# Kernel tuning notes

Hardware: AMD Instinct MI355X
Metric: run time of the kernel (lower is better)

## Reference

```python
import jax, jax.numpy as jnp
import numpy as np

N_NODES = 40000
N_EDGES = 640000
IN_F = 128
HID = 128
N_GRAPHS = 64
N_CLASSES = 2
EPS = 1e-5


def gcn_conv(h_in, W, b, row, col, n):
    # h' = D^-1/2 (A + I) D^-1/2 (X W) + b  (PyG GCNConv with self-loops)
    h = h_in @ W  # [N, out]
    loop = jnp.arange(n, dtype=row.dtype)
    r = jnp.concatenate([row, loop])
    c = jnp.concatenate([col, loop])
    deg = jax.ops.segment_sum(jnp.ones_like(c, dtype=h.dtype), c, num_segments=n)
    dinv = jnp.where(deg > 0, jax.lax.rsqrt(deg), 0.0)
    norm = dinv[r] * dinv[c]  # [E+N]
    msgs = h[r] * norm[:, None]  # gather + scale
    out = jax.ops.segment_sum(msgs, c, num_segments=n)  # scatter-add
    return out + b


def batch_norm(x, gamma, beta):
    mu = jnp.mean(x, axis=0)
    var = jnp.mean(jnp.square(x - mu), axis=0)  # biased, as torch BN
    return gamma * (x - mu) * jax.lax.rsqrt(var + EPS) + beta


def setup_inputs() -> dict:
    key = jax.random.key(0)
    ks = jax.random.split(key, 12)
    s = 1.0 / np.sqrt(HID)
    return {
        "x": jax.random.normal(ks[0], (N_NODES, IN_F), dtype=jnp.float32),
        "edge_index": jax.random.randint(ks[1], (2, N_EDGES), 0, N_NODES, dtype=jnp.int32),
        "batch": jnp.sort(jax.random.randint(ks[2], (N_NODES,), 0, N_GRAPHS, dtype=jnp.int32)),
        "W1": jax.random.normal(ks[3], (IN_F, HID), dtype=jnp.float32) * s,
        "b1": jnp.zeros((HID,), dtype=jnp.float32),
        "W2": jax.random.normal(ks[4], (HID, HID), dtype=jnp.float32) * s,
        "b2": jnp.zeros((HID,), dtype=jnp.float32),
        "gamma1": jnp.ones((HID,), dtype=jnp.float32),
        "beta1": jnp.zeros((HID,), dtype=jnp.float32),
        "gamma2": jnp.ones((HID,), dtype=jnp.float32),
        "beta2": jnp.zeros((HID,), dtype=jnp.float32),
        "lin1_W": jax.random.normal(ks[5], (HID, HID // 2), dtype=jnp.float32) * s,
        "lin1_b": jnp.zeros((HID // 2,), dtype=jnp.float32),
        "lin2_W": jax.random.normal(ks[6], (HID // 2, N_CLASSES), dtype=jnp.float32) * s,
        "lin2_b": jnp.zeros((N_CLASSES,), dtype=jnp.float32),
    }


def reference(x, edge_index, batch, W1, b1, W2, b2, gamma1, beta1, gamma2, beta2,
              lin1_W, lin1_b, lin2_W, lin2_b):
    row, col = edge_index[0], edge_index[1]
    # layer 1: GCNConv -> BN -> ReLU (dropout = identity in eval)
    h = gcn_conv(x, W1, b1, row, col, N_NODES)
    h = jax.nn.relu(batch_norm(h, gamma1, beta1))
    # layer 2
    h = gcn_conv(h, W2, b2, row, col, N_NODES)
    h = jax.nn.relu(batch_norm(h, gamma2, beta2))
    # global mean pool over graphs
    sums = jax.ops.segment_sum(h, batch, num_segments=N_GRAPHS)
    cnt = jax.ops.segment_sum(jnp.ones((N_NODES,), dtype=h.dtype), batch, num_segments=N_GRAPHS)
    pooled = sums / jnp.maximum(cnt, 1.0)[:, None]  # [G, HID]
    z = jax.nn.relu(pooled @ lin1_W + lin1_b)
    return z @ lin2_W + lin2_b  # [G, num_classes]
```

## Files before the change

kernel.cpp:

```cpp
#include <hip/hip_runtime.h>
#include <hip/hip_fp16.h>

#define NN 40000
#define NE 640000
#define F 128
#define NG 64
#define SCAN_NB 157

typedef _Float16 f16x8 __attribute__((ext_vector_type(8)));
typedef float f32x4 __attribute__((ext_vector_type(4)));

union U4H {
    uint4 u;
    f16x8 h;
};

__global__ __launch_bounds__(256) void k_init(const int* __restrict__ batch, int* __restrict__ deg,
                                              float* __restrict__ pooled, float* __restrict__ slabs,
                                              int* __restrict__ gstart, int* __restrict__ gend) {
    int i = blockIdx.x * 256 + threadIdx.x;
    if (i < NN) {
        deg[i] = 0;
        int g = batch[i];
        if (i == 0 || batch[i - 1] != g) gstart[g] = i;
        if (i == NN - 1 || batch[i + 1] != g) gend[g] = i + 1;
    }
    if (i < NG * F) pooled[i] = 0.f;
    if (i < 64 * 128) {
        slabs[i] = 0.f;
        slabs[8192 + i] = 0.f;
        slabs[16384 + i] = 0.f;
        slabs[24576 + i] = 0.f;
    }
}

__global__ __launch_bounds__(256) void k_deg(const int* __restrict__ col, int* __restrict__ deg) {
    int e = blockIdx.x * 256 + threadIdx.x;
    if (e < NE) atomicAdd(&deg[col[e]], 1);
}

__global__ __launch_bounds__(256) void k_scan1(const int* __restrict__ deg, int* __restrict__ partial) {
    __shared__ int sp[256];
    int t = threadIdx.x;
    int i = blockIdx.x * 256 + t;
    sp[t] = (i < NN) ? deg[i] : 0;
    __syncthreads();
#pragma unroll
    for (int off = 128; off > 0; off >>= 1) {
        if (t < off) sp[t] += sp[t + off];
        __syncthreads();
    }
    if (t == 0) partial[blockIdx.x] = sp[0];
}

__global__ __launch_bounds__(256) void k_scan2(const int* __restrict__ partial, int* __restrict__ bsum,
                                               int* __restrict__ indptr) {
    __shared__ int sp[256];
    int t = threadIdx.x;
    int v = (t < SCAN_NB) ? partial[t] : 0;
    sp[t] = v;
    __syncthreads();
#pragma unroll
    for (int off = 1; off < 256; off <<= 1) {
        int add = (t >= off) ? sp[t - off] : 0;
        __syncthreads();
        sp[t] += add;
        __syncthreads();
    }
    if (t < SCAN_NB) bsum[t] = sp[t] - v;
    if (t == SCAN_NB - 1) indptr[NN] = sp[t];
}

__global__ __launch_bounds__(256) void k_scan3(const int* __restrict__ deg, const int* __restrict__ bsum,
                                               int* __restrict__ indptr, int* __restrict__ cursor,
                                               float* __restrict__ dinv) {
    __shared__ int sd[256];
    int t = threadIdx.x;
    int i = blockIdx.x * 256 + t;
    int d = (i < NN) ? deg[i] : 0;
    sd[t] = d;
    __syncthreads();
#pragma unroll
    for (int off = 1; off < 256; off <<= 1) {
        int add = (t >= off) ? sd[t - off] : 0;
        __syncthreads();
        sd[t] += add;
        __syncthreads();
    }
    if (i < NN) {
        int excl = bsum[blockIdx.x] + sd[t] - d;
        indptr[i] = excl;
        cursor[i] = excl;
        dinv[i] = rsqrtf((float)(d + 1));
    }
}

__global__ __launch_bounds__(256) void k_fill(const int* __restrict__ row, const int* __restrict__ col,
                                              int* __restrict__ cursor, int* __restrict__ esrc) {
    int e = blockIdx.x * 256 + threadIdx.x;
    if (e < NE) {
        int c = col[e];
        int slot = atomicAdd(&cursor[c], 1);
        esrc[slot] = row[e];
    }
}

__global__ __launch_bounds__(256) void k_wprep(const float* __restrict__ W1, const float* __restrict__ W2,
                                               _Float16* __restrict__ img1, _Float16* __restrict__ img2) {
    int i = blockIdx.x * 256 + threadIdx.x;
    const float* W = (i < 16384) ? W1 : W2;
    _Float16* img = (i < 16384) ? img1 : img2;
    int j = i & 16383;
    int k = j >> 7, c = j & 127;
    float v = W[j];
    _Float16 h = (_Float16)v;
    _Float16 lo = (_Float16)(v - (float)h);
    int idx = (c * 128 + k) ^ ((c & 7) << 3);
    img[idx] = h;
    img[16384 + idx] = lo;
}

template <int MODE>
__global__ __launch_bounds__(256) void k_mgemm(const void* __restrict__ Ain, const uint4* __restrict__ wimg,
                                               const float* __restrict__ ss, const float* __restrict__ dinv,
                                               unsigned short* __restrict__ G) {
    __shared__ _Float16 WT[2][16384];
    int t = threadIdx.x;
    {
        uint4* dst = (uint4*)&WT[0][0];
#pragma unroll
        for (int i = 0; i < 16; i++) dst[i * 256 + t] = wimg[i * 256 + t];
    }
    __syncthreads();
    int w = t >> 6, l = t & 63;
    int r0w = blockIdx.x * 64 + w * 16;
    int lrow = l & 15, lk = l >> 4;
    int arow = r0w + lrow;

    U4H ah[4], al[4];
    if (MODE == 0) {
        const float* A = (const float*)Ain;
#pragma unroll
        for (int kk = 0; kk < 4; kk++) {
            int k0 = kk * 32 + lk * 8;
            float4 f0 = *(const float4*)&A[arow * 128 + k0];
            float4 f1 = *(const float4*)&A[arow * 128 + k0 + 4];
            float v[8] = {f0.x, f0.y, f0.z, f0.w, f1.x, f1.y, f1.z, f1.w};
#pragma unroll
            for (int j = 0; j < 8; j++) {
                _Float16 h = (_Float16)v[j];
                ah[kk].h[j] = h;
                al[kk].h[j] = (_Float16)(v[j] - (float)h);
            }
        }
    } else {
        const unsigned int* A = (const unsigned int*)Ain;
#pragma unroll
        for (int kk = 0; kk < 4; kk++) {
            int k0 = kk * 32 + lk * 8;
            uint4 u = *(const uint4*)&A[arow * 64 + (k0 >> 1)];
            unsigned int uu[4] = {u.x, u.y, u.z, u.w};
#pragma unroll
            for (int p = 0; p < 4; p++) {
                __half2 hp = *(__half2*)&uu[p];
                int k = k0 + 2 * p;
                float v0 = fmaxf(fmaf(__low2float(hp), ss[k], ss[128 + k]), 0.f);
                float v1 = fmaxf(fmaf(__high2float(hp), ss[k + 1], ss[129 + k]), 0.f);
                _Float16 h0 = (_Float16)v0;
                _Float16 h1 = (_Float16)v1;
                ah[kk].h[2 * p] = h0;
                ah[kk].h[2 * p + 1] = h1;
                al[kk].h[2 * p] = (_Float16)(v0 - (float)h0);
                al[kk].h[2 * p + 1] = (_Float16)(v1 - (float)h1);
            }
        }
    }

    f32x4 acc[8];
#pragma unroll
    for (int ct = 0; ct < 8; ct++) acc[ct] = (f32x4){0.f, 0.f, 0.f, 0.f};

#pragma unroll
    for (int kk = 0; kk < 4; kk++) {
        int k0 = kk * 32 + lk * 8;
#pragma unroll
        for (int ct = 0; ct < 8; ct++) {
            int c = ct * 16 + lrow;
            int idx = (c * 128 + k0) ^ ((c & 7) << 3);
            U4H bh, bl;
            bh.h = *(f16x8*)&WT[0][idx];
            bl.h = *(f16x8*)&WT[1][idx];
            acc[ct] = __builtin_amdgcn_mfma_f32_16x16x32_f16(ah[kk].h, bh.h, acc[ct], 0, 0, 0);
            acc[ct] = __builtin_amdgcn_mfma_f32_16x16x32_f16(al[kk].h, bh.h, acc[ct], 0, 0, 0);
            acc[ct] = __builtin_amdgcn_mfma_f32_16x16x32_f16(ah[kk].h, bl.h, acc[ct], 0, 0, 0);
        }
    }

    float dv[4];
#pragma unroll
    for (int j = 0; j < 4; j++) dv[j] = dinv[r0w + lk * 4 + j];
#pragma unroll
    for (int ct = 0; ct < 8; ct++) {
        int c = ct * 16 + lrow;
#pragma unroll
        for (int j = 0; j < 4; j++) {
            int r = r0w + lk * 4 + j;
            __half hv = __float2half(acc[ct][j] * dv[j]);
            G[r * 128 + c] = *(unsigned short*)&hv;
        }
    }
}

__device__ __forceinline__ void accum8(float* acc, uint4 u) {
    __half2 p0 = *(__half2*)&u.x, p1 = *(__half2*)&u.y, p2 = *(__half2*)&u.z, p3 = *(__half2*)&u.w;
    acc[0] += __low2float(p0); acc[1] += __high2float(p0);
    acc[2] += __low2float(p1); acc[3] += __high2float(p1);
    acc[4] += __low2float(p2); acc[5] += __high2float(p2);
    acc[6] += __low2float(p3); acc[7] += __high2float(p3);
}

__global__ __launch_bounds__(256) void k_agg(const uint4* __restrict__ g16, const int* __restrict__ indptr,
                                             const int* __restrict__ esrc, const float* __restrict__ dinv,
                                             const float* __restrict__ bias, uint4* __restrict__ hout,
                                             float* __restrict__ slabS, float* __restrict__ slabQ) {
    __shared__ float lsS[4][128];
    __shared__ float lsQ[4][128];
    int t = threadIdx.x;
    int w = t >> 6, l = t & 63;
    int slot = l >> 4, lc = l & 15;
    int v = blockIdx.x * 4 + w;
    int s = indptr[v], e = indptr[v + 1];
    float acc[8];
#pragma unroll
    for (int j = 0; j < 8; j++) acc[j] = 0.f;

    int i = s;
    for (; i + 15 < e; i += 16) {
        int r0 = esrc[i + slot];
        int r1 = esrc[i + 4 + slot];
        int r2 = esrc[i + 8 + slot];
        int r3 = esrc[i + 12 + slot];
        uint4 u0 = g16[r0 * 16 + lc];
        uint4 u1 = g16[r1 * 16 + lc];
        uint4 u2 = g16[r2 * 16 + lc];
        uint4 u3 = g16[r3 * 16 + lc];
        accum8(acc, u0);
        accum8(acc, u1);
        accum8(acc, u2);
        accum8(acc, u3);
    }
    for (; i + 3 < e; i += 4) {
        int r0 = esrc[i + slot];
        uint4 u0 = g16[r0 * 16 + lc];
        accum8(acc, u0);
    }
    if (i + slot < e) {
        int r0 = esrc[i + slot];
        uint4 u0 = g16[r0 * 16 + lc];
        accum8(acc, u0);
    }
#pragma unroll
    for (int j = 0; j < 8; j++) {
        acc[j] += __shfl_xor(acc[j], 16, 64);
        acc[j] += __shfl_xor(acc[j], 32, 64);
    }
    if (l < 16) {
        uint4 us = g16[v * 16 + l];
        accum8(acc, us);
        float dvv = dinv[l >= 0 ? v : 0];
        float4 ba = ((const float4*)bias)[2 * l];
        float4 bb = ((const float4*)bias)[2 * l + 1];
        float vv[8];
        vv[0] = acc[0] * dvv + ba.x; vv[1] = acc[1] * dvv + ba.y;
        vv[2] = acc[2] * dvv + ba.z; vv[3] = acc[3] * dvv + ba.w;
        vv[4] = acc[4] * dvv + bb.x; vv[5] = acc[5] * dvv + bb.y;
        vv[6] = acc[6] * dvv + bb.z; vv[7] = acc[7] * dvv + bb.w;
        __half2 h0 = __floats2half2_rn(vv[0], vv[1]);
        __half2 h1 = __floats2half2_rn(vv[2], vv[3]);
        __half2 h2 = __floats2half2_rn(vv[4], vv[5]);
        __half2 h3 = __floats2half2_rn(vv[6], vv[7]);
        uint4 o;
        o.x = *(unsigned int*)&h0; o.y = *(unsigned int*)&h1;
        o.z = *(unsigned int*)&h2; o.w = *(unsigned int*)&h3;
        hout[v * 16 + l] = o;
#pragma unroll
        for (int j = 0; j < 8; j++) {
            lsS[w][l * 8 + j] = vv[j];
            lsQ[w][l * 8 + j] = vv[j] * vv[j];
        }
    }
    __syncthreads();
    int sb = (blockIdx.x & 63) * 128;
    if (t < 128) {
        float v4 = (lsS[0][t] + lsS[1][t]) + (lsS[2][t] + lsS[3][t]);
        atomicAdd(&slabS[sb + t], v4);
    } else {
        int c = t - 128;
        float v4 = (lsQ[0][c] + lsQ[1][c]) + (lsQ[2][c] + lsQ[3][c]);
        atomicAdd(&slabQ[sb + c], v4);
    }
}

__global__ void k_finalize(const float* __restrict__ slabS, const float* __restrict__ slabQ,
                           const float* __restrict__ gamma, const float* __restrict__ beta,
                           float* __restrict__ ss) {
    int c = threadIdx.x;
    float s = 0.f, q = 0.f;
    for (int b = 0; b < 64; b++) {
        s += slabS[b * 128 + c];
        q += slabQ[b * 128 + c];
    }
    float mu = s * (1.f / NN);
    float var = q * (1.f / NN) - mu * mu;
    float sc = gamma[c] * rsqrtf(var + 1e-5f);
    ss[c] = sc;
    ss[128 + c] = beta[c] - mu * sc;
}

__global__ __launch_bounds__(256) void k_pool(const unsigned int* __restrict__ h, const int* __restrict__ batch,
                                              const float* __restrict__ ss, float* __restrict__ pooled) {
    int t = threadIdx.x, c2 = t & 63, q = t >> 6;
    float sc0 = ss[2 * c2], sc1 = ss[2 * c2 + 1];
    float sh0 = ss[128 + 2 * c2], sh1 = ss[129 + 2 * c2];
    int r0 = blockIdx.x * 64;
    int g_cur = -1;
    float a0 = 0.f, a1 = 0.f;
    for (int i = 0; i < 16; i++) {
        int r = r0 + q + 4 * i;
        int g = batch[r];
        unsigned int u = h[r * 64 + c2];
        __half2 p = *(__half2*)&u;
        float v0 = fmaxf(fmaf(__low2float(p), sc0, sh0), 0.f);
        float v1 = fmaxf(fmaf(__high2float(p), sc1, sh1), 0.f);
        if (g != g_cur) {
            if (g_cur >= 0) {
                atomicAdd(&pooled[g_cur * 128 + 2 * c2], a0);
                atomicAdd(&pooled[g_cur * 128 + 2 * c2 + 1], a1);
            }
            a0 = 0.f; a1 = 0.f; g_cur = g;
        }
        a0 += v0; a1 += v1;
    }
    if (g_cur >= 0) {
        atomicAdd(&pooled[g_cur * 128 + 2 * c2], a0);
        atomicAdd(&pooled[g_cur * 128 + 2 * c2 + 1], a1);
    }
}

__global__ __launch_bounds__(256) void k_head(const float* __restrict__ pooled, const int* __restrict__ gstart,
                                              const int* __restrict__ gend, const float* __restrict__ l1W,
                                              const float* __restrict__ l1b, const float* __restrict__ l2W,
                                              const float* __restrict__ l2b, float* __restrict__ out) {
    __shared__ float P[64 * 128];
    __shared__ float Z[64 * 64];
    int t = threadIdx.x;
    for (int i = t; i < 64 * 128; i += 256) {
        int g = i >> 7;
        float cnt = (float)max(gend[g] - gstart[g], 1);
        P[i] = pooled[i] / cnt;
    }
    __syncthreads();
    for (int o = t; o < 64 * 64; o += 256) {
        int g = o >> 6, j = o & 63;
        float s = l1b[j];
        for (int k = 0; k < 128; k++) s += P[g * 128 + k] * l1W[k * 64 + j];
        Z[o] = fmaxf(s, 0.f);
    }
    __syncthreads();
    if (t < 128) {
        int g = t >> 1, cls = t & 1;
        float s = l2b[cls];
        for (int k = 0; k < 64; k++) s += Z[g * 64 + k] * l2W[k * 2 + cls];
        out[g * 2 + cls] = s;
    }
}

extern "C" void kernel_launch(void* const* d_in, const int* in_sizes, int n_in, void* d_out, int out_size,
                              void* d_ws, size_t ws_size, hipStream_t stream) {
    (void)in_sizes; (void)n_in; (void)out_size; (void)ws_size;
    const float* x = (const float*)d_in[0];
    const int* ei = (const int*)d_in[1];
    const int* row = ei;
    const int* col = ei + NE;
    const int* batch = (const int*)d_in[2];
    const float* W1 = (const float*)d_in[3];
    const float* b1 = (const float*)d_in[4];
    const float* W2 = (const float*)d_in[5];
    const float* b2 = (const float*)d_in[6];
    const float* g1 = (const float*)d_in[7];
    const float* be1 = (const float*)d_in[8];
    const float* g2 = (const float*)d_in[9];
    const float* be2 = (const float*)d_in[10];
    const float* l1W = (const float*)d_in[11];
    const float* l1b = (const float*)d_in[12];
    const float* l2W = (const float*)d_in[13];
    const float* l2b = (const float*)d_in[14];
    float* out = (float*)d_out;

    char* ws = (char*)d_ws;
    size_t off = 0;
    auto alloc = [&](size_t bytes) {
        void* p = ws + off;
        off += (bytes + 255) & ~(size_t)255;
        return p;
    };
    unsigned int* g16 = (unsigned int*)alloc(NN * 64 * 4);
    unsigned int* h16a = (unsigned int*)alloc(NN * 64 * 4);
    unsigned int* h16b = (unsigned int*)alloc(NN * 64 * 4);
    int* deg = (int*)alloc(NN * 4);
    float* dinv = (float*)alloc(NN * 4);
    int* indptr = (int*)alloc((NN + 1) * 4);
    int* cursor = (int*)alloc(NN * 4);
    int* esrc = (int*)alloc(NE * 4);
    int* partial = (int*)alloc(256 * 4);
    int* bsum = (int*)alloc(256 * 4);
    float* slabs = (float*)alloc(4 * 64 * 128 * 4);
    float* ss1 = (float*)alloc(256 * 4);
    float* ss2 = (float*)alloc(256 * 4);
    float* pooled = (float*)alloc(NG * F * 4);
    int* gstart = (int*)alloc(NG * 4);
    int* gend = (int*)alloc(NG * 4);
    _Float16* wimg1 = (_Float16*)alloc(32768 * 2);
    _Float16* wimg2 = (_Float16*)alloc(32768 * 2);

    float* slab1S = slabs;
    float* slab1Q = slabs + 8192;
    float* slab2S = slabs + 16384;
    float* slab2Q = slabs + 24576;

    k_init<<<SCAN_NB, 256, 0, stream>>>(batch, deg, pooled, slabs, gstart, gend);
    k_wprep<<<128, 256, 0, stream>>>(W1, W2, wimg1, wimg2);
    k_deg<<<NE / 256, 256, 0, stream>>>(col, deg);
    k_scan1<<<SCAN_NB, 256, 0, stream>>>(deg, partial);
    k_scan2<<<1, 256, 0, stream>>>(partial, bsum, indptr);
    k_scan3<<<SCAN_NB, 256, 0, stream>>>(deg, bsum, indptr, cursor, dinv);
    k_fill<<<NE / 256, 256, 0, stream>>>(row, col, cursor, esrc);

    k_mgemm<0><<<NN / 64, 256, 0, stream>>>(x, (const uint4*)wimg1, nullptr, dinv, (unsigned short*)g16);
    k_agg<<<NN / 4, 256, 0, stream>>>((const uint4*)g16, indptr, esrc, dinv, b1, (uint4*)h16a, slab1S, slab1Q);
    k_finalize<<<1, 128, 0, stream>>>(slab1S, slab1Q, g1, be1, ss1);

    k_mgemm<1><<<NN / 64, 256, 0, stream>>>(h16a, (const uint4*)wimg2, ss1, dinv, (unsigned short*)g16);
    k_agg<<<NN / 4, 256, 0, stream>>>((const uint4*)g16, indptr, esrc, dinv, b2, (uint4*)h16b, slab2S, slab2Q);
    k_finalize<<<1, 128, 0, stream>>>(slab2S, slab2Q, g2, be2, ss2);

    k_pool<<<NN / 64, 256, 0, stream>>>(h16b, batch, ss2, pooled);
    k_head<<<1, 256, 0, stream>>>(pooled, gstart, gend, l1W, l1b, l2W, l2b, out);
}
```

Baseline: 206.6 us.

## Split feature matrices into two 64-column planes and use 16-bit edge sources

The fp16 node-feature buffers are stored as two planes of 64 columns instead of one 128-column row. The aggregation kernel runs twice as many blocks, each handling one plane, with 8 edges per wave step instead of 4. Edge source indices are stored as unsigned short, which halves the CSR index traffic. The aim is a smaller gather working set per pass for better cache locality and more parallelism. The cost is that each edge list is read twice, and node ids above 65535 would break, which is safe only because NN=40000.

```diff
diff --git a/kernel.cpp b/kernel.cpp
--- a/kernel.cpp
+++ b/kernel.cpp
@@ -26,12 +26,7 @@
         if (i == NN - 1 || batch[i + 1] != g) gend[g] = i + 1;
     }
     if (i < NG * F) pooled[i] = 0.f;
-    if (i < 64 * 128) {
-        slabs[i] = 0.f;
-        slabs[8192 + i] = 0.f;
-        slabs[16384 + i] = 0.f;
-        slabs[24576 + i] = 0.f;
-    }
+    if (i < 32768) slabs[i] = 0.f;
 }
 
 __global__ __launch_bounds__(256) void k_deg(const int* __restrict__ col, int* __restrict__ deg) {
@@ -96,12 +91,12 @@
 }
 
 __global__ __launch_bounds__(256) void k_fill(const int* __restrict__ row, const int* __restrict__ col,
-                                              int* __restrict__ cursor, int* __restrict__ esrc) {
+                                              int* __restrict__ cursor, unsigned short* __restrict__ esrc) {
     int e = blockIdx.x * 256 + threadIdx.x;
     if (e < NE) {
         int c = col[e];
         int slot = atomicAdd(&cursor[c], 1);
-        esrc[slot] = row[e];
+        esrc[slot] = (unsigned short)row[e];
     }
 }
 
@@ -154,24 +149,25 @@
             }
         }
     } else {
-        const unsigned int* A = (const unsigned int*)Ain;
+        const uint4* A4 = (const uint4*)Ain;
 #pragma unroll
         for (int kk = 0; kk < 4; kk++) {
             int k0 = kk * 32 + lk * 8;
-            uint4 u = *(const uint4*)&A[arow * 64 + (k0 >> 1)];
+            int p = k0 >> 6, off = (k0 & 63) >> 3;
+            uint4 u = A4[(p * NN + arow) * 8 + off];
             unsigned int uu[4] = {u.x, u.y, u.z, u.w};
 #pragma unroll
-            for (int p = 0; p < 4; p++) {
-                __half2 hp = *(__half2*)&uu[p];
-                int k = k0 + 2 * p;
+            for (int pp = 0; pp < 4; pp++) {
+                __half2 hp = *(__half2*)&uu[pp];
+                int k = k0 + 2 * pp;
                 float v0 = fmaxf(fmaf(__low2float(hp), ss[k], ss[128 + k]), 0.f);
                 float v1 = fmaxf(fmaf(__high2float(hp), ss[k + 1], ss[129 + k]), 0.f);
                 _Float16 h0 = (_Float16)v0;
                 _Float16 h1 = (_Float16)v1;
-                ah[kk].h[2 * p] = h0;
-                ah[kk].h[2 * p + 1] = h1;
-                al[kk].h[2 * p] = (_Float16)(v0 - (float)h0);
-                al[kk].h[2 * p + 1] = (_Float16)(v1 - (float)h1);
+                ah[kk].h[2 * pp] = h0;
+                ah[kk].h[2 * pp + 1] = h1;
+                al[kk].h[2 * pp] = (_Float16)(v0 - (float)h0);
+                al[kk].h[2 * pp + 1] = (_Float16)(v1 - (float)h1);
             }
         }
     }
@@ -202,11 +198,12 @@
 #pragma unroll
     for (int ct = 0; ct < 8; ct++) {
         int c = ct * 16 + lrow;
+        int p = c >> 6, pc = c & 63;
 #pragma unroll
         for (int j = 0; j < 4; j++) {
             int r = r0w + lk * 4 + j;
             __half hv = __float2half(acc[ct][j] * dv[j]);
-            G[r * 128 + c] = *(unsigned short*)&hv;
+            G[(p * NN + r) * 64 + pc] = *(unsigned short*)&hv;
         }
     }
 }
@@ -219,16 +216,21 @@
     acc[6] += __low2float(p3); acc[7] += __high2float(p3);
 }
 
-__global__ __launch_bounds__(256) void k_agg(const uint4* __restrict__ g16, const int* __restrict__ indptr,
-                                             const int* __restrict__ esrc, const float* __restrict__ dinv,
-                                             const float* __restrict__ bias, uint4* __restrict__ hout,
-                                             float* __restrict__ slabS, float* __restrict__ slabQ) {
-    __shared__ float lsS[4][128];
-    __shared__ float lsQ[4][128];
+__global__ __launch_bounds__(256) void k_agg(const uint4* __restrict__ gP, const int* __restrict__ indptr,
+                                             const unsigned short* __restrict__ esrc,
+                                             const float* __restrict__ dinv, const float4* __restrict__ bias4,
+                                             uint4* __restrict__ houtP, float* __restrict__ slabS,
+                                             float* __restrict__ slabQ) {
+    __shared__ float lsS[4][64];
+    __shared__ float lsQ[4][64];
+    int bid = blockIdx.x;
+    int plane = (bid >> 2) & 1;
+    int nodeblk = (bid >> 3) * 4 + (bid & 3);
     int t = threadIdx.x;
     int w = t >> 6, l = t & 63;
-    int slot = l >> 4, lc = l & 15;
-    int v = blockIdx.x * 4 + w;
+    int lc = l & 7, slot = l >> 3;
+    int v = nodeblk * 4 + w;
+    const uint4* gp = gP + plane * (NN * 8);
     int s = indptr[v], e = indptr[v + 1];
     float acc[8];
 #pragma unroll
@@ -237,39 +239,34 @@
     int i = s;
     for (; i + 15 < e; i += 16) {
         int r0 = esrc[i + slot];
-        int r1 = esrc[i + 4 + slot];
-        int r2 = esrc[i + 8 + slot];
-        int r3 = esrc[i + 12 + slot];
-        uint4 u0 = g16[r0 * 16 + lc];
-        uint4 u1 = g16[r1 * 16 + lc];
-        uint4 u2 = g16[r2 * 16 + lc];
-        uint4 u3 = g16[r3 * 16 + lc];
+        int r1 = esrc[i + 8 + slot];
+        uint4 u0 = gp[r0 * 8 + lc];
+        uint4 u1 = gp[r1 * 8 + lc];
         accum8(acc, u0);
         accum8(acc, u1);
-        accum8(acc, u2);
-        accum8(acc, u3);
-    }
-    for (; i + 3 < e; i += 4) {
+    }
+    for (; i + 7 < e; i += 8) {
         int r0 = esrc[i + slot];
-        uint4 u0 = g16[r0 * 16 + lc];
+        uint4 u0 = gp[r0 * 8 + lc];
         accum8(acc, u0);
     }
     if (i + slot < e) {
         int r0 = esrc[i + slot];
-        uint4 u0 = g16[r0 * 16 + lc];
+        uint4 u0 = gp[r0 * 8 + lc];
         accum8(acc, u0);
     }
 #pragma unroll
     for (int j = 0; j < 8; j++) {
+        acc[j] += __shfl_xor(acc[j], 8, 64);
         acc[j] += __shfl_xor(acc[j], 16, 64);
         acc[j] += __shfl_xor(acc[j], 32, 64);
     }
-    if (l < 16) {
-        uint4 us = g16[v * 16 + l];
+    if (slot == 0) {
+        uint4 us = gp[v * 8 + lc];
         accum8(acc, us);
-        float dvv = dinv[l >= 0 ? v : 0];
-        float4 ba = ((const float4*)bias)[2 * l];
-        float4 bb = ((const float4*)bias)[2 * l + 1];
+        float dvv = dinv[v];
+        float4 ba = bias4[plane * 16 + lc * 2];
+        float4 bb = bias4[plane * 16 + lc * 2 + 1];
         float vv[8];
         vv[0] = acc[0] * dvv + ba.x; vv[1] = acc[1] * dvv + ba.y;
         vv[2] = acc[2] * dvv + ba.z; vv[3] = acc[3] * dvv + ba.w;
@@ -282,22 +279,20 @@
         uint4 o;
         o.x = *(unsigned int*)&h0; o.y = *(unsigned int*)&h1;
         o.z = *(unsigned int*)&h2; o.w = *(unsigned int*)&h3;
-        hout[v * 16 + l] = o;
+        houtP[(plane * NN + v) * 8 + lc] = o;
 #pragma unroll
         for (int j = 0; j < 8; j++) {
-            lsS[w][l * 8 + j] = vv[j];
-            lsQ[w][l * 8 + j] = vv[j] * vv[j];
-        }
-    }
-    __syncthreads();
-    int sb = (blockIdx.x & 63) * 128;
-    if (t < 128) {
-        float v4 = (lsS[0][t] + lsS[1][t]) + (lsS[2][t] + lsS[3][t]);
-        atomicAdd(&slabS[sb + t], v4);
-    } else {
-        int c = t - 128;
-        float v4 = (lsQ[0][c] + lsQ[1][c]) + (lsQ[2][c] + lsQ[3][c]);
-        atomicAdd(&slabQ[sb + c], v4);
+            lsS[w][lc * 8 + j] = vv[j];
+            lsQ[w][lc * 8 + j] = vv[j] * vv[j];
+        }
+    }
+    __syncthreads();
+    int sb = plane * 4096 + ((bid >> 3) & 63) * 64;
+    if (t < 64) {
+        atomicAdd(&slabS[sb + t], (lsS[0][t] + lsS[1][t]) + (lsS[2][t] + lsS[3][t]));
+    } else if (t < 128) {
+        int c = t - 64;
+        atomicAdd(&slabQ[sb + c], (lsQ[0][c] + lsQ[1][c]) + (lsQ[2][c] + lsQ[3][c]));
     }
 }
 
@@ -305,10 +300,11 @@
                            const float* __restrict__ gamma, const float* __restrict__ beta,
                            float* __restrict__ ss) {
     int c = threadIdx.x;
+    int plane = c >> 6, col = c & 63;
     float s = 0.f, q = 0.f;
     for (int b = 0; b < 64; b++) {
-        s += slabS[b * 128 + c];
-        q += slabQ[b * 128 + c];
+        s += slabS[plane * 4096 + b * 64 + col];
+        q += slabQ[plane * 4096 + b * 64 + col];
     }
     float mu = s * (1.f / NN);
     float var = q * (1.f / NN) - mu * mu;
@@ -320,6 +316,7 @@
 __global__ __launch_bounds__(256) void k_pool(const unsigned int* __restrict__ h, const int* __restrict__ batch,
                                               const float* __restrict__ ss, float* __restrict__ pooled) {
     int t = threadIdx.x, c2 = t & 63, q = t >> 6;
+    int p = c2 >> 5, pc = c2 & 31;
     float sc0 = ss[2 * c2], sc1 = ss[2 * c2 + 1];
     float sh0 = ss[128 + 2 * c2], sh1 = ss[129 + 2 * c2];
     int r0 = blockIdx.x * 64;
@@ -328,10 +325,10 @@
     for (int i = 0; i < 16; i++) {
         int r = r0 + q + 4 * i;
         int g = batch[r];
-        unsigned int u = h[r * 64 + c2];
-        __half2 p = *(__half2*)&u;
-        float v0 = fmaxf(fmaf(__low2float(p), sc0, sh0), 0.f);
-        float v1 = fmaxf(fmaf(__high2float(p), sc1, sh1), 0.f);
+        unsigned int u = h[(p * NN + r) * 32 + pc];
+        __half2 pr = *(__half2*)&u;
+        float v0 = fmaxf(fmaf(__low2float(pr), sc0, sh0), 0.f);
+        float v1 = fmaxf(fmaf(__high2float(pr), sc1, sh1), 0.f);
         if (g != g_cur) {
             if (g_cur >= 0) {
                 atomicAdd(&pooled[g_cur * 128 + 2 * c2], a0);
@@ -411,10 +408,10 @@
     float* dinv = (float*)alloc(NN * 4);
     int* indptr = (int*)alloc((NN + 1) * 4);
     int* cursor = (int*)alloc(NN * 4);
-    int* esrc = (int*)alloc(NE * 4);
+    unsigned short* esrc = (unsigned short*)alloc(NE * 2);
     int* partial = (int*)alloc(256 * 4);
     int* bsum = (int*)alloc(256 * 4);
-    float* slabs = (float*)alloc(4 * 64 * 128 * 4);
+    float* slabs = (float*)alloc(4 * 8192 * 4);
     float* ss1 = (float*)alloc(256 * 4);
     float* ss2 = (float*)alloc(256 * 4);
     float* pooled = (float*)alloc(NG * F * 4);
@@ -437,11 +434,13 @@
     k_fill<<<NE / 256, 256, 0, stream>>>(row, col, cursor, esrc);
 
     k_mgemm<0><<<NN / 64, 256, 0, stream>>>(x, (const uint4*)wimg1, nullptr, dinv, (unsigned short*)g16);
-    k_agg<<<NN / 4, 256, 0, stream>>>((const uint4*)g16, indptr, esrc, dinv, b1, (uint4*)h16a, slab1S, slab1Q);
+    k_agg<<<NN / 2, 256, 0, stream>>>((const uint4*)g16, indptr, esrc, dinv, (const float4*)b1,
+                                      (uint4*)h16a, slab1S, slab1Q);
     k_finalize<<<1, 128, 0, stream>>>(slab1S, slab1Q, g1, be1, ss1);
 
     k_mgemm<1><<<NN / 64, 256, 0, stream>>>(h16a, (const uint4*)wimg2, ss1, dinv, (unsigned short*)g16);
-    k_agg<<<NN / 4, 256, 0, stream>>>((const uint4*)g16, indptr, esrc, dinv, b2, (uint4*)h16b, slab2S, slab2Q);
+    k_agg<<<NN / 2, 256, 0, stream>>>((const uint4*)g16, indptr, esrc, dinv, (const float4*)b2,
+                                      (uint4*)h16b, slab2S, slab2Q);
     k_finalize<<<1, 128, 0, stream>>>(slab2S, slab2Q, g2, be2, ss2);
 
     k_pool<<<NN / 64, 256, 0, stream>>>(h16b, batch, ss2, pooled);
```

Measured after the change: 217.1 us. 1.05x slower.

## Fuse small setup kernels and BN finalize into neighbors, shrink edge indices

Applied to the files above, without the earlier changes.

Folds the weight-image prep into the init kernel, merges the single-block partial-sum scan into every block of the final scan, and has each GEMM/pool block recompute the BatchNorm scale/shift from the slabs instead of running a separate finalize kernel. This removes four small launches and their serialization gaps. It also stores edge source indices as 16-bit, which halves that gather traffic. The cost is redundant per-block reduction work (64-slab sums in every block). The 16-bit indices rely on node ids fitting in 65535, which holds for 40000 nodes.

```diff
diff --git a/kernel.cpp b/kernel.cpp
--- a/kernel.cpp
+++ b/kernel.cpp
@@ -17,7 +17,9 @@
 
 __global__ __launch_bounds__(256) void k_init(const int* __restrict__ batch, int* __restrict__ deg,
                                               float* __restrict__ pooled, float* __restrict__ slabs,
-                                              int* __restrict__ gstart, int* __restrict__ gend) {
+                                              int* __restrict__ gstart, int* __restrict__ gend,
+                                              const float* __restrict__ W1, const float* __restrict__ W2,
+                                              _Float16* __restrict__ img1, _Float16* __restrict__ img2) {
     int i = blockIdx.x * 256 + threadIdx.x;
     if (i < NN) {
         deg[i] = 0;
@@ -26,11 +28,18 @@
         if (i == NN - 1 || batch[i + 1] != g) gend[g] = i + 1;
     }
     if (i < NG * F) pooled[i] = 0.f;
-    if (i < 64 * 128) {
-        slabs[i] = 0.f;
-        slabs[8192 + i] = 0.f;
-        slabs[16384 + i] = 0.f;
-        slabs[24576 + i] = 0.f;
+    if (i < 32768) slabs[i] = 0.f;
+    if (i < 32768) {
+        const float* W = (i < 16384) ? W1 : W2;
+        _Float16* img = (i < 16384) ? img1 : img2;
+        int j = i & 16383;
+        int k = j >> 7, c = j & 127;
+        float v = W[j];
+        _Float16 h = (_Float16)v;
+        _Float16 lo = (_Float16)(v - (float)h);
+        int idx = (c * 128 + k) ^ ((c & 7) << 3);
+        img[idx] = h;
+        img[16384 + idx] = lo;
     }
 }
 
@@ -53,12 +62,13 @@
     if (t == 0) partial[blockIdx.x] = sp[0];
 }
 
-__global__ __launch_bounds__(256) void k_scan2(const int* __restrict__ partial, int* __restrict__ bsum,
-                                               int* __restrict__ indptr) {
+__global__ __launch_bounds__(256) void k_scan3(const int* __restrict__ deg, const int* __restrict__ partial,
+                                               int* __restrict__ indptr, int* __restrict__ cursor,
+                                               float* __restrict__ dinv) {
     __shared__ int sp[256];
-    int t = threadIdx.x;
-    int v = (t < SCAN_NB) ? partial[t] : 0;
-    sp[t] = v;
+    __shared__ int sd[256];
+    int t = threadIdx.x;
+    sp[t] = (t < SCAN_NB) ? partial[t] : 0;
     __syncthreads();
 #pragma unroll
     for (int off = 1; off < 256; off <<= 1) {
@@ -67,16 +77,11 @@
         sp[t] += add;
         __syncthreads();
     }
-    if (t < SCAN_NB) bsum[t] = sp[t] - v;
-    if (t == SCAN_NB - 1) indptr[NN] = sp[t];
-}
-
-__global__ __launch_bounds__(256) void k_scan3(const int* __restrict__ deg, const int* __restrict__ bsum,
-                                               int* __restrict__ indptr, int* __restrict__ cursor,
-                                               float* __restrict__ dinv) {
-    __shared__ int sd[256];
-    int t = threadIdx.x;
-    int i = blockIdx.x * 256 + t;
+    int bid = blockIdx.x;
+    if (bid == 0 && t == 0) indptr[NN] = sp[SCAN_NB - 1];
+    int bsum = (bid == 0) ? 0 : sp[bid - 1];
+
+    int i = bid * 256 + t;
     int d = (i < NN) ? deg[i] : 0;
     sd[t] = d;
     __syncthreads();
@@ -88,7 +93,7 @@
         __syncthreads();
     }
     if (i < NN) {
-        int excl = bsum[blockIdx.x] + sd[t] - d;
+        int excl = bsum + sd[t] - d;
         indptr[i] = excl;
         cursor[i] = excl;
         dinv[i] = rsqrtf((float)(d + 1));
@@ -96,40 +101,39 @@
 }
 
 __global__ __launch_bounds__(256) void k_fill(const int* __restrict__ row, const int* __restrict__ col,
-                                              int* __restrict__ cursor, int* __restrict__ esrc) {
+                                              int* __restrict__ cursor, unsigned short* __restrict__ esrc) {
     int e = blockIdx.x * 256 + threadIdx.x;
     if (e < NE) {
         int c = col[e];
         int slot = atomicAdd(&cursor[c], 1);
-        esrc[slot] = row[e];
-    }
-}
-
-__global__ __launch_bounds__(256) void k_wprep(const float* __restrict__ W1, const float* __restrict__ W2,
-                                               _Float16* __restrict__ img1, _Float16* __restrict__ img2) {
-    int i = blockIdx.x * 256 + threadIdx.x;
-    const float* W = (i < 16384) ? W1 : W2;
-    _Float16* img = (i < 16384) ? img1 : img2;
-    int j = i & 16383;
-    int k = j >> 7, c = j & 127;
-    float v = W[j];
-    _Float16 h = (_Float16)v;
-    _Float16 lo = (_Float16)(v - (float)h);
-    int idx = (c * 128 + k) ^ ((c & 7) << 3);
-    img[idx] = h;
-    img[16384 + idx] = lo;
+        esrc[slot] = (unsigned short)row[e];
+    }
 }
 
 template <int MODE>
 __global__ __launch_bounds__(256) void k_mgemm(const void* __restrict__ Ain, const uint4* __restrict__ wimg,
-                                               const float* __restrict__ ss, const float* __restrict__ dinv,
-                                               unsigned short* __restrict__ G) {
+                                               const float* __restrict__ slabS, const float* __restrict__ slabQ,
+                                               const float* __restrict__ gamma, const float* __restrict__ beta,
+                                               const float* __restrict__ dinv, unsigned short* __restrict__ G) {
     __shared__ _Float16 WT[2][16384];
+    __shared__ float ssl[256];
     int t = threadIdx.x;
     {
         uint4* dst = (uint4*)&WT[0][0];
 #pragma unroll
         for (int i = 0; i < 16; i++) dst[i * 256 + t] = wimg[i * 256 + t];
+    }
+    if (MODE == 1 && t < 128) {
+        float s = 0.f, q = 0.f;
+        for (int b = 0; b < 64; b++) {
+            s += slabS[b * 128 + t];
+            q += slabQ[b * 128 + t];
+        }
+        float mu = s * (1.f / NN);
+        float var = q * (1.f / NN) - mu * mu;
+        float sc = gamma[t] * rsqrtf(var + 1e-5f);
+        ssl[t] = sc;
+        ssl[128 + t] = beta[t] - mu * sc;
     }
     __syncthreads();
     int w = t >> 6, l = t & 63;
@@ -164,8 +168,8 @@
             for (int p = 0; p < 4; p++) {
                 __half2 hp = *(__half2*)&uu[p];
                 int k = k0 + 2 * p;
-                float v0 = fmaxf(fmaf(__low2float(hp), ss[k], ss[128 + k]), 0.f);
-                float v1 = fmaxf(fmaf(__high2float(hp), ss[k + 1], ss[129 + k]), 0.f);
+                float v0 = fmaxf(fmaf(__low2float(hp), ssl[k], ssl[128 + k]), 0.f);
+                float v1 = fmaxf(fmaf(__high2float(hp), ssl[k + 1], ssl[129 + k]), 0.f);
                 _Float16 h0 = (_Float16)v0;
                 _Float16 h1 = (_Float16)v1;
                 ah[kk].h[2 * p] = h0;
@@ -220,9 +224,10 @@
 }
 
 __global__ __launch_bounds__(256) void k_agg(const uint4* __restrict__ g16, const int* __restrict__ indptr,
-                                             const int* __restrict__ esrc, const float* __restrict__ dinv,
-                                             const float* __restrict__ bias, uint4* __restrict__ hout,
-                                             float* __restrict__ slabS, float* __restrict__ slabQ) {
+                                             const unsigned short* __restrict__ esrc,
+                                             const float* __restrict__ dinv, const float4* __restrict__ bias4,
+                                             uint4* __restrict__ hout, float* __restrict__ slabS,
+                                             float* __restrict__ slabQ) {
     __shared__ float lsS[4][128];
     __shared__ float lsQ[4][128];
     int t = threadIdx.x;
@@ -267,9 +272,9 @@
     if (l < 16) {
         uint4 us = g16[v * 16 + l];
         accum8(acc, us);
-        float dvv = dinv[l >= 0 ? v : 0];
-        float4 ba = ((const float4*)bias)[2 * l];
-        float4 bb = ((const float4*)bias)[2 * l + 1];
+        float dvv = dinv[v];
+        float4 ba = bias4[2 * l];
+        float4 bb = bias4[2 * l + 1];
         float vv[8];
         vv[0] = acc[0] * dvv + ba.x; vv[1] = acc[1] * dvv + ba.y;
         vv[2] = acc[2] * dvv + ba.z; vv[3] = acc[3] * dvv + ba.w;
@@ -292,36 +297,35 @@
     __syncthreads();
     int sb = (blockIdx.x & 63) * 128;
     if (t < 128) {
-        float v4 = (lsS[0][t] + lsS[1][t]) + (lsS[2][t] + lsS[3][t]);
-        atomicAdd(&slabS[sb + t], v4);
+        atomicAdd(&slabS[sb + t], (lsS[0][t] + lsS[1][t]) + (lsS[2][t] + lsS[3][t]));
     } else {
         int c = t - 128;
-        float v4 = (lsQ[0][c] + lsQ[1][c]) + (lsQ[2][c] + lsQ[3][c]);
-        atomicAdd(&slabQ[sb + c], v4);
-    }
-}
-
-__global__ void k_finalize(const float* __restrict__ slabS, const float* __restrict__ slabQ,
-                           const float* __restrict__ gamma, const float* __restrict__ beta,
-                           float* __restrict__ ss) {
-    int c = threadIdx.x;
-    float s = 0.f, q = 0.f;
-    for (int b = 0; b < 64; b++) {
-        s += slabS[b * 128 + c];
-        q += slabQ[b * 128 + c];
-    }
-    float mu = s * (1.f / NN);
-    float var = q * (1.f / NN) - mu * mu;
-    float sc = gamma[c] * rsqrtf(var + 1e-5f);
-    ss[c] = sc;
-    ss[128 + c] = beta[c] - mu * sc;
+        atomicAdd(&slabQ[sb + c], (lsQ[0][c] + lsQ[1][c]) + (lsQ[2][c] + lsQ[3][c]));
+    }
 }
 
 __global__ __launch_bounds__(256) void k_pool(const unsigned int* __restrict__ h, const int* __restrict__ batch,
-                                              const float* __restrict__ ss, float* __restrict__ pooled) {
-    int t = threadIdx.x, c2 = t & 63, q = t >> 6;
-    float sc0 = ss[2 * c2], sc1 = ss[2 * c2 + 1];
-    float sh0 = ss[128 + 2 * c2], sh1 = ss[129 + 2 * c2];
+                                              const float* __restrict__ slabS, const float* __restrict__ slabQ,
+                                              const float* __restrict__ gamma, const float* __restrict__ beta,
+                                              float* __restrict__ pooled) {
+    __shared__ float ssl[256];
+    int t = threadIdx.x;
+    if (t < 128) {
+        float s = 0.f, q = 0.f;
+        for (int b = 0; b < 64; b++) {
+            s += slabS[b * 128 + t];
+            q += slabQ[b * 128 + t];
+        }
+        float mu = s * (1.f / NN);
+        float var = q * (1.f / NN) - mu * mu;
+        float sc = gamma[t] * rsqrtf(var + 1e-5f);
+        ssl[t] = sc;
+        ssl[128 + t] = beta[t] - mu * sc;
+    }
+    __syncthreads();
+    int c2 = t & 63, q = t >> 6;
+    float sc0 = ssl[2 * c2], sc1 = ssl[2 * c2 + 1];
+    float sh0 = ssl[128 + 2 * c2], sh1 = ssl[129 + 2 * c2];
     int r0 = blockIdx.x * 64;
     int g_cur = -1;
     float a0 = 0.f, a1 = 0.f;
@@ -411,12 +415,9 @@
     float* dinv = (float*)alloc(NN * 4);
     int* indptr = (int*)alloc((NN + 1) * 4);
     int* cursor = (int*)alloc(NN * 4);
-    int* esrc = (int*)alloc(NE * 4);
+    unsigned short* esrc = (unsigned short*)alloc(NE * 2);
     int* partial = (int*)alloc(256 * 4);
-    int* bsum = (int*)alloc(256 * 4);
-    float* slabs = (float*)alloc(4 * 64 * 128 * 4);
-    float* ss1 = (float*)alloc(256 * 4);
-    float* ss2 = (float*)alloc(256 * 4);
+    float* slabs = (float*)alloc(4 * 8192 * 4);
     float* pooled = (float*)alloc(NG * F * 4);
     int* gstart = (int*)alloc(NG * 4);
     int* gend = (int*)alloc(NG * 4);
@@ -428,22 +429,22 @@
     float* slab2S = slabs + 16384;
     float* slab2Q = slabs + 24576;
 
-    k_init<<<SCAN_NB, 256, 0, stream>>>(batch, deg, pooled, slabs, gstart, gend);
-    k_wprep<<<128, 256, 0, stream>>>(W1, W2, wimg1, wimg2);
+    k_init<<<SCAN_NB, 256, 0, stream>>>(batch, deg, pooled, slabs, gstart, gend, W1, W2, wimg1, wimg2);
     k_deg<<<NE / 256, 256, 0, stream>>>(col, deg);
     k_scan1<<<SCAN_NB, 256, 0, stream>>>(deg, partial);
-    k_scan2<<<1, 256, 0, stream>>>(partial, bsum, indptr);
-    k_scan3<<<SCAN_NB, 256, 0, stream>>>(deg, bsum, indptr, cursor, dinv);
+    k_scan3<<<SCAN_NB, 256, 0, stream>>>(deg, partial, indptr, cursor, dinv);
     k_fill<<<NE / 256, 256, 0, stream>>>(row, col, cursor, esrc);
 
-    k_mgemm<0><<<NN / 64, 256, 0, stream>>>(x, (const uint4*)wimg1, nullptr, dinv, (unsigned short*)g16);
-    k_agg<<<NN / 4, 256, 0, stream>>>((const uint4*)g16, indptr, esrc, dinv, b1, (uint4*)h16a, slab1S, slab1Q);
-    k_finalize<<<1, 128, 0, stream>>>(slab1S, slab1Q, g1, be1, ss1);
-
-    k_mgemm<1><<<NN / 64, 256, 0, stream>>>(h16a, (const uint4*)wimg2, ss1, dinv, (unsigned short*)g16);
-    k_agg<<<NN / 4, 256, 0, stream>>>((const uint4*)g16, indptr, esrc, dinv, b2, (uint4*)h16b, slab2S, slab2Q);
-    k_finalize<<<1, 128, 0, stream>>>(slab2S, slab2Q, g2, be2, ss2);
-
-    k_pool<<<NN / 64, 256, 0, stream>>>(h16b, batch, ss2, pooled);
+    k_mgemm<0><<<NN / 64, 256, 0, stream>>>(x, (const uint4*)wimg1, nullptr, nullptr, nullptr, nullptr, dinv,
+                                            (unsigned short*)g16);
+    k_agg<<<NN / 4, 256, 0, stream>>>((const uint4*)g16, indptr, esrc, dinv, (const float4*)b1, (uint4*)h16a,
+                                      slab1S, slab1Q);
+
+    k_mgemm<1><<<NN / 64, 256, 0, stream>>>(h16a, (const uint4*)wimg2, slab1S, slab1Q, g1, be1, dinv,
+                                            (unsigned short*)g16);
+    k_agg<<<NN / 4, 256, 0, stream>>>((const uint4*)g16, indptr, esrc, dinv, (const float4*)b2, (uint4*)h16b,
+                                      slab2S, slab2Q);
+
+    k_pool<<<NN / 64, 256, 0, stream>>>(h16b, batch, slab2S, slab2Q, g2, be2, pooled);
     k_head<<<1, 256, 0, stream>>>(pooled, gstart, gend, l1W, l1b, l2W, l2b, out);
 }
```

After: 195.5 us. -5.4%, faster.
